# Optimization experiments

Hardware: AMD Instinct MI355X
Metric: run time of the kernel (lower is better)

Reference implementation:

```python
import jax, jax.numpy as jnp
import numpy as np

B, D, S, E = 256, 5, 30, 768
H1, H2, FF, OUT = 512, 512, 256, 2


def setup_inputs() -> dict:
    key = jax.random.key(0)
    ks = iter(jax.random.split(key, 40))

    def p(shape, scale=0.05):
        return jax.random.normal(next(ks), shape, jnp.float32) * scale

    return {
        "sentence_feats": jax.random.normal(next(ks), (B, D, S, E), jnp.float32),
        "time_feats": jax.random.uniform(next(ks), (B, D, S), jnp.float32),
        "len_tweets": jax.random.randint(next(ks), (B, D), 1, S + 1, jnp.int32),
        # TimeLSTM (lstm1)
        "Wd_w": p((H1, H1)), "Wd_b": p((H1,)),
        "Wall_w": p((4 * H1, H1)), "Wall_b": p((4 * H1,)),
        "Uall_w": p((4 * H1, E)), "Uall_b": p((4 * H1,)),
        # attn1
        "A1_W1_w": p((H1, H1)), "A1_W1_b": p((H1,)),
        "A1_W2_w": p((H1, H1)), "A1_W2_b": p((H1,)),
        "A1_V_w": p((1, H1)), "A1_V_b": p((1,)),
        # nn.LSTM (lstm2), gate order i,f,g,o
        "L2_Wih": p((4 * H2, H1)), "L2_Whh": p((4 * H2, H2)),
        "L2_bih": p((4 * H2,)), "L2_bhh": p((4 * H2,)),
        # attn2
        "A2_W1_w": p((H2, H2)), "A2_W1_b": p((H2,)),
        "A2_W2_w": p((H2, H2)), "A2_W2_b": p((H2,)),
        "A2_V_w": p((1, H2)), "A2_V_b": p((1,)),
        # head
        "lin3_w": p((FF, H2)), "lin3_b": p((FF,)),
        "lin4_w": p((OUT, FF)), "lin4_b": p((OUT,)),
    }


def _time_lstm(x, t, Wd_w, Wd_b, Wall_w, Wall_b, Uall_w, Uall_b):
    # x: (N,S,E), t: (N,S) -> o-gate outputs (N,S,H) (the torch module stacks `o`, not `h`)
    N = x.shape[0]
    H = Wd_w.shape[0]
    ux = jnp.einsum('nse,ge->nsg', x, Uall_w) + Uall_b  # (N,S,4H), hoisted out of recurrence

    def step(carry, inp):
        h, c = carry
        ux_s, t_s = inp
        c_s1 = jnp.tanh(c @ Wd_w.T + Wd_b)
        c_adj = c - c_s1 + c_s1 * t_s[:, None]
        gates = jax.nn.sigmoid(h @ Wall_w.T + Wall_b + ux_s)
        f, i, o, c_tmp = jnp.split(gates, 4, axis=1)  # all sigmoid, incl. c_tmp (as in source)
        c = f * c_adj + i * c_tmp
        h = o * jnp.tanh(c)
        return (h, c), o

    init = (jnp.zeros((N, H), x.dtype), jnp.zeros((N, H), x.dtype))
    _, os = jax.lax.scan(step, init, (ux.transpose(1, 0, 2), t.T))
    return os.transpose(1, 0, 2)  # (N,S,H)


def _std_lstm(x, Wih, Whh, bih, bhh):
    # PyTorch nn.LSTM, 1 layer, batch_first. x: (B,T,I) -> (hs (B,T,H), h_n (B,H))
    Bn = x.shape[0]
    H = Whh.shape[1]
    xi = jnp.einsum('bti,gi->btg', x, Wih) + bih + bhh  # (B,T,4H)

    def step(carry, xi_t):
        h, c = carry
        g = xi_t + h @ Whh.T
        i, f, gg, o = jnp.split(g, 4, axis=1)
        c = jax.nn.sigmoid(f) * c + jax.nn.sigmoid(i) * jnp.tanh(gg)
        h = jax.nn.sigmoid(o) * jnp.tanh(c)
        return (h, c), h

    init = (jnp.zeros((Bn, H), x.dtype), jnp.zeros((Bn, H), x.dtype))
    (h_n, _), hs = jax.lax.scan(step, init, xi.transpose(1, 0, 2))
    return hs.transpose(1, 0, 2), h_n


def _forward(sentence_feats, time_feats, Wd_w, Wd_b, Wall_w, Wall_b, Uall_w, Uall_b,
             A1_W1_w, A1_W1_b, A1_W2_w, A1_W2_b, A1_V_w, A1_V_b,
             L2_Wih, L2_Whh, L2_bih, L2_bhh,
             A2_W1_w, A2_W1_b, A2_W2_w, A2_W2_b, A2_V_w, A2_V_b,
             lin3_w, lin3_b, lin4_w, lin4_b, len_tweets):
    x = sentence_feats.transpose(1, 0, 2, 3)  # (D,B,S,E)
    t = time_feats.transpose(1, 0, 2)         # (D,B,S)
    lens = len_tweets.transpose(1, 0)          # (D,B)
    d, b, s, e = x.shape

    # run TimeLSTM over all days at once (days are independent, shared zero init)
    outs = _time_lstm(x.reshape(d * b, s, e), t.reshape(d * b, s),
                      Wd_w, Wd_b, Wall_w, Wall_b, Uall_w, Uall_b).reshape(d, b, s, H1)

    # Faithful to the source's inner loop: temp_hn ends up as the LAST batch
    # element's output at index len-1, shared across the whole batch of that day.
    idx = lens[:, -1] - 1  # (D,)
    last = jnp.take_along_axis(outs[:, -1], idx[:, None, None], axis=1)[:, 0]  # (D,H1)

    # attn1: score = V(tanh(W1(last) + W2(full))), mask by lens, softmax over S
    s1 = jnp.tanh((last @ A1_W1_w.T + A1_W1_b)[:, None, None, :]
                  + jnp.einsum('dbsh,gh->dbsg', outs, A1_W2_w) + A1_W2_b)
    score = jnp.einsum('dbsh,oh->dbso', s1, A1_V_w) + A1_V_b  # (D,B,S,1)
    mask = jnp.arange(s)[None, None, :] < lens[:, :, None]     # (D,B,S)
    score = jnp.where(mask[..., None], score, -jnp.inf)
    aw = jax.nn.softmax(score, axis=2)
    lstm1_out = jnp.sum(aw * outs, axis=2).transpose(1, 0, 2)  # (B,D,H1)

    lstm2_out, hn2 = _std_lstm(lstm1_out, L2_Wih, L2_Whh, L2_bih, L2_bhh)  # (B,D,H2),(B,H2)

    # attn2 over days
    s2 = jnp.tanh((hn2 @ A2_W1_w.T + A2_W1_b)[:, None, :]
                  + lstm2_out @ A2_W2_w.T + A2_W2_b)
    score2 = s2 @ A2_V_w.T + A2_V_b                 # (B,D,1)
    aw2 = jax.nn.softmax(score2, axis=1)
    ctx = jnp.sum(aw2 * lstm2_out, axis=1)          # (B,H2)

    h3 = jax.nn.relu(ctx @ lin3_w.T + lin3_b)       # dropout = identity (eval mode)
    return h3 @ lin4_w.T + lin4_b                   # (B,OUT)


def reference(sentence_feats, time_feats, len_tweets, Wd_w, Wd_b, Wall_w, Wall_b, Uall_w, Uall_b,
              A1_W1_w, A1_W1_b, A1_W2_w, A1_W2_b, A1_V_w, A1_V_b,
              L2_Wih, L2_Whh, L2_bih, L2_bhh,
              A2_W1_w, A2_W1_b, A2_W2_w, A2_W2_b, A2_V_w, A2_V_b,
              lin3_w, lin3_b, lin4_w, lin4_b):
    return _forward(sentence_feats, time_feats, Wd_w, Wd_b, Wall_w, Wall_b, Uall_w, Uall_b,
                    A1_W1_w, A1_W1_b, A1_W2_w, A1_W2_b, A1_V_w, A1_V_b,
                    L2_Wih, L2_Whh, L2_bih, L2_bhh,
                    A2_W1_w, A2_W1_b, A2_W2_w, A2_W2_b, A2_V_w, A2_V_b,
                    lin3_w, lin3_b, lin4_w, lin4_b, len_tweets)
```

## Files before the change

kernel.cpp:

```cpp
#include <hip/hip_runtime.h>
#include <math.h>

typedef _Float16 f16;
typedef _Float16 f16x4 __attribute__((ext_vector_type(4)));
typedef _Float16 f16x8 __attribute__((ext_vector_type(8)));
typedef float f32x4 __attribute__((ext_vector_type(4)));

#define DEV static __device__ __forceinline__

#define OFF_X16    ((size_t)0)
#define OFF_UX     ((size_t)58982400)
#define OFF_OUTS   ((size_t)216268800)
#define OFF_WD     ((size_t)255590400)
#define OFF_WALLP  ((size_t)256114688)
#define OFF_UP     ((size_t)258211840)
#define OFF_W2     ((size_t)261357568)
#define OFF_WIHP   ((size_t)261881856)
#define OFF_WHHP   ((size_t)263979008)
#define OFF_A2W1C  ((size_t)266076160)
#define OFF_A2W2C  ((size_t)266600448)
#define OFF_L3WC   ((size_t)267124736)
#define OFF_BALLP  ((size_t)267386880)
#define OFF_BIHP   ((size_t)267395072)
#define OFF_H16    ((size_t)267403264)
#define OFF_C16    ((size_t)270024704)
#define OFF_C32    ((size_t)272646144)
#define WS_NEED    ((size_t)277889024)
#define OFF_SCORE  ((size_t)0)
#define OFF_W1L    ((size_t)153600)
#define OFF_L1O32  ((size_t)163840)
#define OFF_L1O16  ((size_t)2785280)
#define OFF_XI2    ((size_t)4096000)
#define OFF_C2     ((size_t)14581760)
#define OFF_H2     ((size_t)15630336)
#define OFF_L2O32  ((size_t)16154624)
#define OFF_L2O16  ((size_t)18776064)
#define OFF_U2     ((size_t)20086784)
#define OFF_V2     ((size_t)22708224)
#define OFF_CTX16  ((size_t)23232512)
#define OFF_H3     ((size_t)23494656)
#define OFF_TFT    ((size_t)23756800)

DEV float sigf(float x) { return 1.f / (1.f + __expf(-x)); }
DEV float tanhfast(float x) { float e = __expf(2.f * x); return 1.f - 2.f / (e + 1.f); }
DEV int permrow(int c) { return (((c >> 4) & 3) << 9) | ((c >> 6) << 4) | (c & 15); }

DEV void gload16(const f16* g, f16x8* lds) {
  __builtin_amdgcn_global_load_lds((const __attribute__((address_space(1))) void*)g,
                                   (__attribute__((address_space(3))) void*)lds, 16, 0, 0);
}

DEV void gemm_core(const f16* __restrict__ A, const f16* __restrict__ Bt, int K,
                   int rowBase, int colBase, f16x8* sh, f32x4 (&acc)[4][4]) {
  const int t = threadIdx.x, lane = t & 63, w = t >> 6;
  const int wr = (w >> 1) * 64, wc = (w & 1) * 64;
  const f16* Arow = A + (size_t)rowBase * K;
  const f16* Brow = Bt + (size_t)colBase * K;
  auto stage = [&](f16x8* dstBase, const f16* src, int k0) {
#pragma unroll
    for (int i = 0; i < 4; ++i) {
      int c = i * 256 + t; int r = c >> 3; int cc = (c & 7) ^ (r & 7);
      gload16(src + (size_t)r * K + (k0 + cc * 8), dstBase + i * 256 + (t & 192));
    }
  };
  stage(sh, Arow, 0);
  stage(sh + 2048, Brow, 0);
  const int nk = K >> 6;
  for (int kt = 0; kt < nk; ++kt) {
    const int cur = kt & 1;
    if (kt + 1 < nk) {
      stage(sh + (cur ^ 1) * 1024, Arow, (kt + 1) * 64);
      stage(sh + 2048 + (cur ^ 1) * 1024, Brow, (kt + 1) * 64);
      asm volatile("s_waitcnt vmcnt(8)" ::: "memory");
    } else {
      asm volatile("s_waitcnt vmcnt(0)" ::: "memory");
    }
    __builtin_amdgcn_s_barrier();
    __builtin_amdgcn_sched_barrier(0);
    const f16x8* shA = sh + cur * 1024;
    const f16x8* shB = sh + 2048 + cur * 1024;
    const int rr = lane & 15, chb = lane >> 4;
#pragma unroll
    for (int kk = 0; kk < 2; ++kk) {
      const int ch = kk * 4 + chb;
      f16x8 af[4], bf[4];
#pragma unroll
      for (int m = 0; m < 4; ++m) { int row = wr + m * 16 + rr; af[m] = shA[row * 8 + (ch ^ (row & 7))]; }
#pragma unroll
      for (int n = 0; n < 4; ++n) { int row = wc + n * 16 + rr; bf[n] = shB[row * 8 + (ch ^ (row & 7))]; }
#pragma unroll
      for (int m = 0; m < 4; ++m)
#pragma unroll
        for (int n = 0; n < 4; ++n)
          acc[m][n] = __builtin_amdgcn_mfma_f32_16x16x32_f16(af[m], bf[n], acc[m][n], 0, 0, 0);
    }
    __builtin_amdgcn_sched_barrier(0);
    __builtin_amdgcn_s_barrier();
  }
}

DEV void gemm_core256(const f16* __restrict__ A, const f16* __restrict__ Bt, int K,
                      int rowBase, int colBase, f16x8 (&shA)[2][2048], f16x8 (&shB)[2][2048],
                      f32x4 (&acc)[8][4]) {
  const int t = threadIdx.x, lane = t & 63, w = t >> 6;
  const int wm = w >> 2, wn = w & 3;
  const f16* Arow = A + (size_t)rowBase * K;
  const f16* Brow = Bt + (size_t)colBase * K;
  auto stage = [&](f16x8* dst, const f16* src, int k0) {
#pragma unroll
    for (int i = 0; i < 4; ++i) {
      int c = i * 512 + t; int r = c >> 3; int cc = (c & 7) ^ (r & 7);
      gload16(src + (size_t)r * K + (k0 + cc * 8), dst + i * 512 + (t & 448));
    }
  };
  stage(shA[0], Arow, 0);
  stage(shB[0], Brow, 0);
  const int nk = K >> 6;
  for (int kt = 0; kt < nk; ++kt) {
    const int cur = kt & 1;
    if (kt + 1 < nk) {
      stage(shA[cur ^ 1], Arow, (kt + 1) * 64);
      stage(shB[cur ^ 1], Brow, (kt + 1) * 64);
      asm volatile("s_waitcnt vmcnt(8)" ::: "memory");
    } else {
      asm volatile("s_waitcnt vmcnt(0)" ::: "memory");
    }
    __builtin_amdgcn_s_barrier();
    __builtin_amdgcn_sched_barrier(0);
    const f16x8* pA = shA[cur];
    const f16x8* pB = shB[cur];
    const int rr = lane & 15, chb = lane >> 4;
#pragma unroll
    for (int kk = 0; kk < 2; ++kk) {
      const int ch = kk * 4 + chb;
      f16x8 bf[4];
#pragma unroll
      for (int n = 0; n < 4; ++n) { int row = wn * 64 + n * 16 + rr; bf[n] = pB[row * 8 + (ch ^ (row & 7))]; }
#pragma unroll
      for (int m = 0; m < 8; ++m) {
        int row = wm * 128 + m * 16 + rr;
        f16x8 af = pA[row * 8 + (ch ^ (row & 7))];
#pragma unroll
        for (int n = 0; n < 4; ++n)
          acc[m][n] = __builtin_amdgcn_mfma_f32_16x16x32_f16(af, bf[n], acc[m][n], 0, 0, 0);
      }
    }
    __builtin_amdgcn_sched_barrier(0);
    __builtin_amdgcn_s_barrier();
  }
}

__global__ __launch_bounds__(512, 1) void k_gemm256(const f16* __restrict__ A, const f16* __restrict__ Bt,
                                                    int K, int N, f16* __restrict__ C16) {
  __shared__ f16x8 shA[2][2048];
  __shared__ f16x8 shB[2][2048];
  const int rb = blockIdx.y * 256, cb = blockIdx.x * 256;
  f32x4 acc[8][4] = {};
  gemm_core256(A, Bt, K, rb, cb, shA, shB, acc);
  const int t = threadIdx.x, lane = t & 63, w = t >> 6;
  const int wm = w >> 2, wn = w & 3;
  const int ec = lane & 15, er = (lane >> 4) * 4;
#pragma unroll
  for (int m = 0; m < 8; ++m)
#pragma unroll
    for (int n = 0; n < 4; ++n) {
      const int c = cb + wn * 64 + n * 16 + ec;
#pragma unroll
      for (int j = 0; j < 4; ++j) {
        const int r = rb + wm * 128 + m * 16 + er + j;
        C16[(size_t)r * N + c] = (f16)acc[m][n][j];
      }
    }
}

__global__ __launch_bounds__(512, 1) void k_score2(const f16* __restrict__ outs, const f16* __restrict__ W2t,
    const float* __restrict__ W2b, const float* __restrict__ w1l, const float* __restrict__ V,
    float* __restrict__ score) {
  __shared__ f16x8 shA[2][2048];
  __shared__ f16x8 shB[2][2048];
  __shared__ float sacc[256];
  const int rb = blockIdx.y * 256, cb = blockIdx.x * 256;
  f32x4 acc[8][4] = {};
  gemm_core256(outs, W2t, 512, rb, cb, shA, shB, acc);
  const int t = threadIdx.x, lane = t & 63, w = t >> 6;
  const int wm = w >> 2, wn = w & 3;
  const int ec = lane & 15, er = (lane >> 4) * 4;
  if (t < 256) sacc[t] = 0.f;
  __syncthreads();
#pragma unroll
  for (int m = 0; m < 8; ++m)
#pragma unroll
    for (int j = 0; j < 4; ++j) {
      const int lr = wm * 128 + m * 16 + er + j;
      const int r = rb + lr;
      const int d = (r / 30) >> 8;
      float p = 0.f;
#pragma unroll
      for (int n = 0; n < 4; ++n) {
        const int c = cb + wn * 64 + n * 16 + ec;
        p += V[c] * tanhfast(acc[m][n][j] + W2b[c] + w1l[d * 512 + c]);
      }
      p += __shfl_xor(p, 1); p += __shfl_xor(p, 2); p += __shfl_xor(p, 4); p += __shfl_xor(p, 8);
      if (ec == 0) atomicAdd(&sacc[lr], p);
    }
  __syncthreads();
  if (t < 256) atomicAdd(&score[rb + t], sacc[t]);
}

template <int ACT, bool O32, bool O16>
__global__ __launch_bounds__(256, 2) void k_gemm(const f16* __restrict__ A, const f16* __restrict__ Bt,
                                                 int K, int N, const float* __restrict__ bias,
                                                 float* __restrict__ C32, f16* __restrict__ C16) {
  __shared__ f16x8 sh[4096];
  const int rb = blockIdx.y * 128, cb = blockIdx.x * 128;
  f32x4 acc[4][4] = {};
  gemm_core(A, Bt, K, rb, cb, sh, acc);
  const int t = threadIdx.x, lane = t & 63, w = t >> 6;
  const int wr = (w >> 1) * 64, wc = (w & 1) * 64, ec = lane & 15, er = (lane >> 4) * 4;
#pragma unroll
  for (int m = 0; m < 4; ++m)
#pragma unroll
    for (int n = 0; n < 4; ++n) {
      const int c = cb + wc + n * 16 + ec;
      const float bv = bias ? bias[c] : 0.f;
#pragma unroll
      for (int j = 0; j < 4; ++j) {
        const int r = rb + wr + m * 16 + er + j;
        float v = acc[m][n][j] + bv;
        if (ACT == 3) v = fmaxf(v, 0.f);
        if (O32) C32[(size_t)r * N + c] = v;
        if (O16) C16[(size_t)r * N + c] = (f16)v;
      }
    }
}

__global__ __launch_bounds__(256, 1) void k_stepf(
    const f16* __restrict__ hin, const f16* __restrict__ cin16, const float* __restrict__ cin32,
    const f16* __restrict__ Wallp, const f16* __restrict__ Wd16,
    const f16* __restrict__ ux, const float* __restrict__ ballp, const float* __restrict__ Wd_b,
    const float* __restrict__ tft,
    float* __restrict__ cout32, f16* __restrict__ cout16, f16* __restrict__ hout,
    f16* __restrict__ outs, int s) {
  __shared__ f16x8 shA[2048];
  __shared__ f16x8 shB[2048];
  __shared__ f16x8 shC[2048];
  __shared__ f16x8 shD[512];
  __shared__ f16x8 shU[2048];
  __shared__ f16x8 shE[1024];
  const int t = threadIdx.x, lane = t & 63, w = t >> 6;
  const int rb = ((int)blockIdx.x >> 4) * 128;
  const int cg = (int)blockIdx.x & 15;
  const int wr = (w >> 1) * 64, wc = (w & 1) * 64;
  const int rr = lane & 15, chb = lane >> 4;
  const int ec = lane & 15, er = (lane >> 4) * 4;
  const int h = cg * 32 + (w & 1) * 16 + ec;
  const int hcol = (w & 1) * 16 + ec;
  const f16* Ah = hin + (size_t)rb * 512;
  const f16* Ac = cin16 + (size_t)rb * 512;
  const f16* Bw = Wallp + (size_t)cg * 128 * 512;
  const f16* Bd = Wd16 + (size_t)cg * 32 * 512;
  float bW[4];
#pragma unroll
  for (int n = 0; n < 4; ++n) bW[n] = ballp[cg * 128 + wc + n * 16 + ec];
  const float bD = Wd_b[h];
  const f16* shUf = (const f16*)shU;
  const float* shEf = (const float*)shE;
  const int kbase = (wc >> 3) + (ec >> 3);
  f32x4 acc[4][4] = {};
  f32x4 acc2[4] = {};

  auto stage128 = [&](f16x8* dstBase, const f16* src, int k0) {
#pragma unroll
    for (int i = 0; i < 4; ++i) {
      int c = i * 256 + t; int r = c >> 3; int cc = (c & 7) ^ (r & 7);
      gload16(src + (size_t)r * 512 + (k0 + cc * 8), dstBase + i * 256 + (t & 192));
    }
  };
  auto stage32 = [&](f16x8* dstBase, const f16* src, int k0) {
    const int r = t >> 3; const int cc = (t & 7) ^ (r & 7);
    gload16(src + (size_t)r * 512 + (k0 + cc * 8), dstBase + (t & 192));
  };
  auto stageU = [&]() {
#pragma unroll
    for (int i = 0; i < 8; ++i) {
      int c = i * 256 + t; int lr = c >> 4; int k = c & 15;
      int klog = k ^ (((lr >> 2) & 3) << 1);
      gload16(ux + ((size_t)(rb + lr) * 30 + s) * 2048 + cg * 128 + klog * 8,
              shU + i * 256 + (t & 192));
    }
  };
  auto stageE = [&]() {
#pragma unroll
    for (int i = 0; i < 4; ++i) {
      int c = i * 256 + t; int lr = c >> 3; int k = c & 7;
      int klog = k ^ (((lr >> 2) & 1) << 2);
      gload16((const f16*)(cin32 + (size_t)(rb + lr) * 512 + cg * 32 + klog * 4),
              shE + i * 256 + (t & 192));
    }
  };

  if (s == 0) {
    stageU();
    stageE();
    asm volatile("s_waitcnt vmcnt(0)" ::: "memory");
    __builtin_amdgcn_s_barrier();
  } else {
    stage128(shA, Ah, 0);
    stage128(shB, Bw, 0);
    stage128(shC, Ac, 0);
    stage32(shD, Bd, 0);
    stageU();
    stageE();
    for (int kt = 0; kt < 8; ++kt) {
      const int cur = kt & 1;
      if (kt < 7) {
        stage128(shA + (cur ^ 1) * 1024, Ah, (kt + 1) * 64);
        stage128(shB + (cur ^ 1) * 1024, Bw, (kt + 1) * 64);
        stage128(shC + (cur ^ 1) * 1024, Ac, (kt + 1) * 64);
        stage32(shD + (cur ^ 1) * 256, Bd, (kt + 1) * 64);
        asm volatile("s_waitcnt vmcnt(13)" ::: "memory");
      } else {
        asm volatile("s_waitcnt vmcnt(0)" ::: "memory");
      }
      __builtin_amdgcn_s_barrier();
      __builtin_amdgcn_sched_barrier(0);
      const f16x8* pA = shA + cur * 1024;
      const f16x8* pB = shB + cur * 1024;
      const f16x8* pC = shC + cur * 1024;
      const f16x8* pD = shD + cur * 256;
#pragma unroll
      for (int kk = 0; kk < 2; ++kk) {
        const int ch = kk * 4 + chb;
        f16x8 af[4], bf[4], cf[4], df;
#pragma unroll
        for (int m = 0; m < 4; ++m) {
          const int row = wr + m * 16 + rr;
          af[m] = pA[row * 8 + (ch ^ (row & 7))];
          cf[m] = pC[row * 8 + (ch ^ (row & 7))];
        }
#pragma unroll
        for (int n = 0; n < 4; ++n) { const int row = wc + n * 16 + rr; bf[n] = pB[row * 8 + (ch ^ (row & 7))]; }
        { const int row = (w & 1) * 16 + rr; df = pD[row * 8 + (ch ^ (row & 7))]; }
#pragma unroll
        for (int m = 0; m < 4; ++m) {
#pragma unroll
          for (int n = 0; n < 4; ++n)
            acc[m][n] = __builtin_amdgcn_mfma_f32_16x16x32_f16(af[m], bf[n], acc[m][n], 0, 0, 0);
          acc2[m] = __builtin_amdgcn_mfma_f32_16x16x32_f16(cf[m], df, acc2[m], 0, 0, 0);
        }
      }
      __builtin_amdgcn_sched_barrier(0);
      __builtin_amdgcn_s_barrier();
    }
  }

#pragma unroll
  for (int m = 0; m < 4; ++m)
#pragma unroll
    for (int j = 0; j < 4; ++j) {
      const int lr = wr + m * 16 + er + j;
      const int r = rb + lr;
      const float tv = tft[s * 1280 + r];
      const int sU = ((lr >> 2) & 3) << 1;
      const float u0 = (float)shUf[(lr * 16 + ((kbase + 0) ^ sU)) * 8 + (ec & 7)];
      const float u1 = (float)shUf[(lr * 16 + ((kbase + 2) ^ sU)) * 8 + (ec & 7)];
      const float u2v = (float)shUf[(lr * 16 + ((kbase + 4) ^ sU)) * 8 + (ec & 7)];
      const float u3 = (float)shUf[(lr * 16 + ((kbase + 6) ^ sU)) * 8 + (ec & 7)];
      const float p0 = acc[m][0][j] + bW[0] + u0;
      const float p1 = acc[m][1][j] + bW[1] + u1;
      const float p2 = acc[m][2][j] + bW[2] + u2v;
      const float p3 = acc[m][3][j] + bW[3] + u3;
      const float f = sigf(p0), i = sigf(p1), o = sigf(p2), ct = sigf(p3);
      const float cs = tanhfast(acc2[m][j] + bD);
      const int sE = ((lr >> 2) & 1) << 2;
      const float c_old = shEf[(lr * 8 + ((hcol >> 2) ^ sE)) * 4 + (hcol & 3)];
      const float cadj = c_old - cs + cs * tv;
      const float cn = f * cadj + i * ct;
      cout32[(size_t)r * 512 + h] = cn;
      cout16[(size_t)r * 512 + h] = (f16)cn;
      hout[(size_t)r * 512 + h] = (f16)(o * tanhfast(cn));
      outs[((size_t)r * 30 + s) * 512 + h] = (f16)o;
    }
}

__global__ __launch_bounds__(256, 2) void k_l2step(const f16* __restrict__ hin, const f16* __restrict__ Whhp,
    const float* __restrict__ xi2, const float* __restrict__ cin, float* __restrict__ cout,
    f16* __restrict__ hout, float* __restrict__ l2o32, f16* __restrict__ l2o16, int ts) {
  __shared__ f16x8 sh[4096];
  const int rb = (blockIdx.x >> 4) * 128, cg = blockIdx.x & 15;
  f32x4 acc[4][4] = {};
  gemm_core(hin, Whhp, 512, rb, cg * 128, sh, acc);
  const int t = threadIdx.x, lane = t & 63, w = t >> 6;
  const int wr = (w >> 1) * 64, wc = (w & 1) * 64, ec = lane & 15, er = (lane >> 4) * 4;
  const int h = cg * 32 + (w & 1) * 16 + ec;
#pragma unroll
  for (int m = 0; m < 4; ++m)
#pragma unroll
    for (int j = 0; j < 4; ++j) {
      const int r = rb + wr + m * 16 + er + j;
      const size_t xb = ((size_t)r * 5 + ts) * 2048 + cg * 128 + wc + ec;
      const float p0 = acc[m][0][j] + xi2[xb];
      const float p1 = acc[m][1][j] + xi2[xb + 16];
      const float p2 = acc[m][2][j] + xi2[xb + 32];
      const float p3 = acc[m][3][j] + xi2[xb + 48];
      const float ii = sigf(p0), ff = sigf(p1), gg = tanhfast(p2), oo = sigf(p3);
      const float cn = ff * cin[(size_t)r * 512 + h] + ii * gg;
      const float hn = oo * tanhfast(cn);
      cout[(size_t)r * 512 + h] = cn;
      hout[(size_t)r * 512 + h] = (f16)hn;
      const size_t ob = ((size_t)r * 5 + ts) * 512 + h;
      l2o32[ob] = hn;
      l2o16[ob] = (f16)hn;
    }
}

__global__ __launch_bounds__(256) void k_w1last(const f16* __restrict__ outs, const int* __restrict__ lens,
                                                const float* __restrict__ W1, const float* __restrict__ W1b,
                                                float* __restrict__ w1l) {
  __shared__ float lastv[512];
  const int d = blockIdx.x;
  const int idx = lens[255 * 5 + d] - 1;
  const size_t row = ((size_t)(d * 256 + 255) * 30 + idx) * 512;
  for (int h = threadIdx.x; h < 512; h += 256) lastv[h] = (float)outs[row + h];
  __syncthreads();
  for (int h = threadIdx.x; h < 512; h += 256) {
    const float* wr = W1 + (size_t)h * 512;
    float p = W1b[h];
    for (int k = 0; k < 512; ++k) p += lastv[k] * wr[k];
    w1l[d * 512 + h] = p;
  }
}

__global__ __launch_bounds__(256) void k_attn1(const float* __restrict__ score, const f16* __restrict__ outs,
                                               const int* __restrict__ lens,
                                               float* __restrict__ l1o32, f16* __restrict__ l1o16) {
  __shared__ float saw[32];
  const int n = blockIdx.x;
  const int d = n >> 8, b = n & 255;
  const int len = lens[b * 5 + d];
  const int t = threadIdx.x, lane = t & 63, w = t >> 6;
  if (w == 0) {
    const bool valid = lane < len;
    float sc = valid ? score[(size_t)n * 30 + lane] : -INFINITY;
    float mx = sc;
#pragma unroll
    for (int off = 32; off > 0; off >>= 1) mx = fmaxf(mx, __shfl_xor(mx, off));
    float e = valid ? __expf(sc - mx) : 0.f;
    float sm = e;
#pragma unroll
    for (int off = 32; off > 0; off >>= 1) sm += __shfl_xor(sm, off);
    if (lane < 30) saw[lane] = e / sm;
  }
  __syncthreads();
  for (int h = t; h < 512; h += 256) {
    float acc = 0.f;
    for (int s = 0; s < len; ++s) acc += saw[s] * (float)outs[((size_t)n * 30 + s) * 512 + h];
    const size_t o = ((size_t)b * 5 + d) * 512 + h;
    l1o32[o] = acc;
    l1o16[o] = (f16)acc;
  }
}

__global__ __launch_bounds__(256, 2) void k_uv(const f16* __restrict__ l2o16, const f16* __restrict__ A2W2c,
    const f16* __restrict__ h2fin, const f16* __restrict__ A2W1c,
    const float* __restrict__ bu, const float* __restrict__ bv,
    float* __restrict__ u2, float* __restrict__ v2) {
  __shared__ f16x8 sh[4096];
  const int bid = blockIdx.x;
  const f16* A; const f16* B; const float* bias; float* out; int rb, cb;
  if (bid < 40) { A = l2o16; B = A2W2c; bias = bu; out = u2; rb = (bid >> 2) * 128; cb = (bid & 3) * 128; }
  else { int b2 = bid - 40; A = h2fin; B = A2W1c; bias = bv; out = v2; rb = (b2 >> 2) * 128; cb = (b2 & 3) * 128; }
  f32x4 acc[4][4] = {};
  gemm_core(A, B, 512, rb, cb, sh, acc);
  const int t = threadIdx.x, lane = t & 63, w = t >> 6;
  const int wr = (w >> 1) * 64, wc = (w & 1) * 64, ec = lane & 15, er = (lane >> 4) * 4;
#pragma unroll
  for (int m = 0; m < 4; ++m)
#pragma unroll
    for (int n = 0; n < 4; ++n) {
      const int c = cb + wc + n * 16 + ec;
      const float bvv = bias[c];
#pragma unroll
      for (int j = 0; j < 4; ++j) out[(size_t)(rb + wr + m * 16 + er + j) * 512 + c] = acc[m][n][j] + bvv;
    }
}

__global__ __launch_bounds__(256) void k_attn2(const float* __restrict__ u2, const float* __restrict__ v2,
                                               const float* __restrict__ l2o, const float* __restrict__ V2,
                                               const float* __restrict__ V2b, f16* __restrict__ ctx16) {
  __shared__ float ssc[8];
  __shared__ float saw[8];
  const int b = blockIdx.x;
  const int t = threadIdx.x, lane = t & 63, w = t >> 6;
  for (int tt = w; tt < 5; tt += 4) {
    const float* ur = u2 + ((size_t)b * 5 + tt) * 512;
    const float* vr = v2 + (size_t)b * 512;
    float p = 0.f;
#pragma unroll
    for (int j = 0; j < 8; ++j) { int h = lane * 8 + j; p += V2[h] * tanhfast(ur[h] + vr[h]); }
#pragma unroll
    for (int off = 32; off > 0; off >>= 1) p += __shfl_down(p, off);
    if (lane == 0) ssc[tt] = p + V2b[0];
  }
  __syncthreads();
  if (w == 0) {
    const bool valid = lane < 5;
    float sc = valid ? ssc[lane] : -INFINITY;
    float mx = sc;
#pragma unroll
    for (int off = 32; off > 0; off >>= 1) mx = fmaxf(mx, __shfl_xor(mx, off));
    float e = valid ? __expf(sc - mx) : 0.f;
    float sm = e;
#pragma unroll
    for (int off = 32; off > 0; off >>= 1) sm += __shfl_xor(sm, off);
    if (valid) saw[lane] = e / sm;
  }
  __syncthreads();
  for (int h = t; h < 512; h += 256) {
    float a = 0.f;
#pragma unroll
    for (int tt = 0; tt < 5; ++tt) a += saw[tt] * l2o[((size_t)b * 5 + tt) * 512 + h];
    ctx16[(size_t)b * 512 + h] = (f16)a;
  }
}

__global__ __launch_bounds__(256) void k_final(const float* __restrict__ h3, const float* __restrict__ W4,
                                               const float* __restrict__ b4, float* __restrict__ out) {
  const int idx = blockIdx.x * 256 + threadIdx.x;
  const int b = idx >> 1, o = idx & 1;
  const float* hr = h3 + b * 256;
  const float* wr = W4 + o * 256;
  float p = b4[o];
  for (int j = 0; j < 256; ++j) p += hr[j] * wr[j];
  out[idx] = p;
}

__global__ __launch_bounds__(256) void k_castx(const float* __restrict__ sf, f16* __restrict__ x16) {
  const int total = 7372800;
  for (int e = blockIdx.x * 256 + threadIdx.x; e < total; e += gridDim.x * 256) {
    const int row = e / 192, k = e - row * 192;
    const int b = row / 150, rem = row - b * 150;
    const int d = rem / 30, s = rem - d * 30;
    const int orow = (d * 256 + b) * 30 + s;
    const float4 v = ((const float4*)sf)[e];
    f16x4 o = {(f16)v.x, (f16)v.y, (f16)v.z, (f16)v.w};
    ((f16x4*)x16)[(size_t)orow * 192 + k] = o;
  }
}

struct WPArgs { const float* src[9]; f16* dst[9]; int k4[9]; int cnt4[9]; int perm[9]; };
__global__ __launch_bounds__(256) void k_castwp(WPArgs a) {
  int g = blockIdx.x * 256 + threadIdx.x;
#pragma unroll
  for (int si = 0; si < 9; ++si) {
    if (g < a.cnt4[si]) {
      const int K4 = a.k4[si];
      const int c = g / K4, k = g - c * K4;
      const int srow = a.perm[si] ? permrow(c) : c;
      const float4 v = ((const float4*)a.src[si])[(size_t)srow * K4 + k];
      f16x4 o = {(f16)v.x, (f16)v.y, (f16)v.z, (f16)v.w};
      ((f16x4*)a.dst[si])[(size_t)c * K4 + k] = o;
      return;
    }
    g -= a.cnt4[si];
  }
}

__global__ __launch_bounds__(256) void k_zero(f16* h16a, f16* c16a, float* c32a,
    float* ballp, float* bihp, const float* Wall_b, const float* Uall_b,
    const float* bih, const float* bhh, float* tft, const float* tf,
    float* score, const float* Vb, f16* h2a, float* c2a) {
  const int i = blockIdx.x * 256 + threadIdx.x;
  if (i < 655360) { h16a[i] = (f16)0.f; c16a[i] = (f16)0.f; c32a[i] = 0.f; }
  if (i < 2048) {
    const int p = permrow(i);
    ballp[i] = Wall_b[p] + Uall_b[p];
    bihp[i] = bih[p] + bhh[p];
  }
  if (i < 38400) {
    const int s = i / 1280, r = i - s * 1280;
    const int d = r >> 8, b = r & 255;
    tft[i] = tf[((size_t)b * 5 + d) * 30 + s];
    score[i] = Vb[0];
  }
  if (i < 131072) { h2a[i] = (f16)0.f; c2a[i] = 0.f; }
}

extern "C" void kernel_launch(void* const* d_in, const int* in_sizes, int n_in,
                              void* d_out, int out_size, void* d_ws, size_t ws_size,
                              hipStream_t stream) {
  const float* sf     = (const float*)d_in[0];
  const float* tf     = (const float*)d_in[1];
  const int*   lens   = (const int*)d_in[2];
  const float* Wd_w   = (const float*)d_in[3];
  const float* Wd_b   = (const float*)d_in[4];
  const float* Wall_w = (const float*)d_in[5];
  const float* Wall_b = (const float*)d_in[6];
  const float* Uall_w = (const float*)d_in[7];
  const float* Uall_b = (const float*)d_in[8];
  const float* A1W1   = (const float*)d_in[9];
  const float* A1W1b  = (const float*)d_in[10];
  const float* A1W2   = (const float*)d_in[11];
  const float* A1W2b  = (const float*)d_in[12];
  const float* A1V    = (const float*)d_in[13];
  const float* A1Vb   = (const float*)d_in[14];
  const float* Wih    = (const float*)d_in[15];
  const float* Whh    = (const float*)d_in[16];
  const float* bih    = (const float*)d_in[17];
  const float* bhh    = (const float*)d_in[18];
  const float* A2W1   = (const float*)d_in[19];
  const float* A2W1b  = (const float*)d_in[20];
  const float* A2W2   = (const float*)d_in[21];
  const float* A2W2b  = (const float*)d_in[22];
  const float* A2V    = (const float*)d_in[23];
  const float* A2Vb   = (const float*)d_in[24];
  const float* L3w    = (const float*)d_in[25];
  const float* L3b    = (const float*)d_in[26];
  const float* L4w    = (const float*)d_in[27];
  const float* L4b    = (const float*)d_in[28];

  if (ws_size < WS_NEED) return;
  char* ws = (char*)d_ws;
  f16*   x16    = (f16*)(ws + OFF_X16);
  f16*   ux16   = (f16*)(ws + OFF_UX);
  f16*   outs16 = (f16*)(ws + OFF_OUTS);
  f16*   Wd16   = (f16*)(ws + OFF_WD);
  f16*   Wallp  = (f16*)(ws + OFF_WALLP);
  f16*   U16p   = (f16*)(ws + OFF_UP);
  f16*   W216   = (f16*)(ws + OFF_W2);
  f16*   Wihp   = (f16*)(ws + OFF_WIHP);
  f16*   Whhp   = (f16*)(ws + OFF_WHHP);
  f16*   A2W116 = (f16*)(ws + OFF_A2W1C);
  f16*   A2W216 = (f16*)(ws + OFF_A2W2C);
  f16*   L316   = (f16*)(ws + OFF_L3WC);
  float* ballp  = (float*)(ws + OFF_BALLP);
  float* bihp   = (float*)(ws + OFF_BIHP);
  f16*   h16b[2]  = {(f16*)(ws + OFF_H16), (f16*)(ws + OFF_H16 + 1310720)};
  f16*   c16b[2]  = {(f16*)(ws + OFF_C16), (f16*)(ws + OFF_C16 + 1310720)};
  float* c32b[2]  = {(float*)(ws + OFF_C32), (float*)(ws + OFF_C32 + 2621440)};
  float* score  = (float*)(ws + OFF_SCORE);
  float* w1l    = (float*)(ws + OFF_W1L);
  float* l1o32  = (float*)(ws + OFF_L1O32);
  f16*   l1o16  = (f16*)(ws + OFF_L1O16);
  float* xi2    = (float*)(ws + OFF_XI2);
  float* c2b[2] = {(float*)(ws + OFF_C2), (float*)(ws + OFF_C2 + 524288)};
  f16*   h2b[2] = {(f16*)(ws + OFF_H2), (f16*)(ws + OFF_H2 + 262144)};
  float* l2o32  = (float*)(ws + OFF_L2O32);
  f16*   l2o16  = (f16*)(ws + OFF_L2O16);
  float* u2     = (float*)(ws + OFF_U2);
  float* v2     = (float*)(ws + OFF_V2);
  f16*   ctx16  = (f16*)(ws + OFF_CTX16);
  float* h3     = (float*)(ws + OFF_H3);
  float* tft    = (float*)(ws + OFF_TFT);

  k_castx<<<2048, 256, 0, stream>>>(sf, x16);
  WPArgs wa;
  wa.src[0] = Wd_w;   wa.dst[0] = Wd16;   wa.k4[0] = 128; wa.cnt4[0] = 65536;  wa.perm[0] = 0;
  wa.src[1] = A1W2;   wa.dst[1] = W216;   wa.k4[1] = 128; wa.cnt4[1] = 65536;  wa.perm[1] = 0;
  wa.src[2] = A2W1;   wa.dst[2] = A2W116; wa.k4[2] = 128; wa.cnt4[2] = 65536;  wa.perm[2] = 0;
  wa.src[3] = A2W2;   wa.dst[3] = A2W216; wa.k4[3] = 128; wa.cnt4[3] = 65536;  wa.perm[3] = 0;
  wa.src[4] = L3w;    wa.dst[4] = L316;   wa.k4[4] = 128; wa.cnt4[4] = 32768;  wa.perm[4] = 0;
  wa.src[5] = Wall_w; wa.dst[5] = Wallp;  wa.k4[5] = 128; wa.cnt4[5] = 262144; wa.perm[5] = 1;
  wa.src[6] = Uall_w; wa.dst[6] = U16p;   wa.k4[6] = 192; wa.cnt4[6] = 393216; wa.perm[6] = 1;
  wa.src[7] = Wih;    wa.dst[7] = Wihp;   wa.k4[7] = 128; wa.cnt4[7] = 262144; wa.perm[7] = 1;
  wa.src[8] = Whh;    wa.dst[8] = Whhp;   wa.k4[8] = 128; wa.cnt4[8] = 262144; wa.perm[8] = 1;
  k_castwp<<<5760, 256, 0, stream>>>(wa);

  k_gemm256<<<dim3(8, 150), 512, 0, stream>>>(x16, U16p, 768, 2048, ux16);

  k_zero<<<2560, 256, 0, stream>>>(h16b[0], c16b[0], c32b[0], ballp, bihp, Wall_b, Uall_b, bih, bhh,
                                   tft, tf, score, A1Vb, h2b[0], c2b[0]);

  for (int s = 0; s < 30; ++s) {
    const int pi = s & 1, po = pi ^ 1;
    k_stepf<<<160, 256, 0, stream>>>(h16b[pi], c16b[pi], c32b[pi], Wallp, Wd16, ux16, ballp, Wd_b, tft,
                                     c32b[po], c16b[po], h16b[po], outs16, s);
  }

  k_w1last<<<5, 256, 0, stream>>>(outs16, lens, A1W1, A1W1b, w1l);
  k_score2<<<dim3(2, 150), 512, 0, stream>>>(outs16, W216, A1W2b, w1l, A1V, score);
  k_attn1<<<1280, 256, 0, stream>>>(score, outs16, lens, l1o32, l1o16);

  k_gemm<0, true, false><<<dim3(16, 10), 256, 0, stream>>>(l1o16, Wihp, 512, 2048, bihp, xi2, nullptr);
  for (int ts = 0; ts < 5; ++ts) {
    const int pi = ts & 1, po = pi ^ 1;
    k_l2step<<<32, 256, 0, stream>>>(h2b[pi], Whhp, xi2, c2b[pi], c2b[po], h2b[po], l2o32, l2o16, ts);
  }

  k_uv<<<48, 256, 0, stream>>>(l2o16, A2W216, h2b[1], A2W116, A2W2b, A2W1b, u2, v2);
  k_attn2<<<256, 256, 0, stream>>>(u2, v2, l2o32, A2V, A2Vb, ctx16);

  k_gemm<3, true, false><<<dim3(2, 2), 256, 0, stream>>>(ctx16, L316, 512, 256, L3b, h3, nullptr);
  k_final<<<2, 256, 0, stream>>>(h3, L4w, L4b, (float*)d_out);
}
```

Before: 1.016 ms.

## Overlap input projection GEMM with TimeLSTM recurrence steps

The x·Uᵀ projection is no longer computed in full before the recurrence. The input is re-laid out time-major, only the first two timesteps' slabs are computed up front, and each recurrence launch adds 160 extra blocks that compute slab s+2 alongside the step. This hides most of the large projection GEMM behind the latency-bound, underfilled recurrence kernels. The cost is shared LDS allocation, heavier launches, and moving the tft/score/h2 buffers to avoid aliasing with the workspace.

```diff
diff --git a/kernel.cpp b/kernel.cpp
--- a/kernel.cpp
+++ b/kernel.cpp
@@ -25,8 +25,9 @@
 #define OFF_H16    ((size_t)267403264)
 #define OFF_C16    ((size_t)270024704)
 #define OFF_C32    ((size_t)272646144)
-#define WS_NEED    ((size_t)277889024)
-#define OFF_SCORE  ((size_t)0)
+#define OFF_TFTN   ((size_t)277889024)
+#define OFF_SCOREN (OFF_TFTN + 153600)
+#define WS_NEED    (OFF_SCOREN + 153600)
 #define OFF_W1L    ((size_t)153600)
 #define OFF_L1O32  ((size_t)163840)
 #define OFF_L1O16  ((size_t)2785280)
@@ -39,7 +40,6 @@
 #define OFF_V2     ((size_t)22708224)
 #define OFF_CTX16  ((size_t)23232512)
 #define OFF_H3     ((size_t)23494656)
-#define OFF_TFT    ((size_t)23756800)
 
 DEV float sigf(float x) { return 1.f / (1.f + __expf(-x)); }
 DEV float tanhfast(float x) { float e = __expf(2.f * x); return 1.f - 2.f / (e + 1.f); }
@@ -234,31 +234,55 @@
     }
 }
 
-__global__ __launch_bounds__(256, 1) void k_stepf(
+__global__ __launch_bounds__(256, 1) void k_stepm(
     const f16* __restrict__ hin, const f16* __restrict__ cin16, const float* __restrict__ cin32,
     const f16* __restrict__ Wallp, const f16* __restrict__ Wd16,
     const f16* __restrict__ ux, const float* __restrict__ ballp, const float* __restrict__ Wd_b,
     const float* __restrict__ tft,
     float* __restrict__ cout32, f16* __restrict__ cout16, f16* __restrict__ hout,
-    f16* __restrict__ outs, int s) {
-  __shared__ f16x8 shA[2048];
-  __shared__ f16x8 shB[2048];
-  __shared__ f16x8 shC[2048];
-  __shared__ f16x8 shD[512];
-  __shared__ f16x8 shU[2048];
-  __shared__ f16x8 shE[1024];
-  const int t = threadIdx.x, lane = t & 63, w = t >> 6;
-  const int rb = ((int)blockIdx.x >> 4) * 128;
-  const int cg = (int)blockIdx.x & 15;
+    f16* __restrict__ outs,
+    const f16* __restrict__ x16s, const f16* __restrict__ U16p, f16* __restrict__ uxout, int s) {
+  __shared__ f16x8 shAll[9728];
+  const int bid = (int)blockIdx.x;
+  const int t = threadIdx.x, lane = t & 63, w = t >> 6;
   const int wr = (w >> 1) * 64, wc = (w & 1) * 64;
+  const int ec = lane & 15, er = (lane >> 4) * 4;
+
+  if (bid >= 160) {
+    const int q = bid - 160;
+    const int slab = s + 2;
+    const int rbu = (q >> 4) * 128, cbu = (q & 15) * 128;
+    f32x4 acc[4][4] = {};
+    gemm_core(x16s + (size_t)slab * 1280 * 768, U16p, 768, rbu, cbu, shAll, acc);
+    f16* C = uxout + (size_t)slab * 1280 * 2048;
+#pragma unroll
+    for (int m = 0; m < 4; ++m)
+#pragma unroll
+      for (int n = 0; n < 4; ++n) {
+        const int c = cbu + wc + n * 16 + ec;
+#pragma unroll
+        for (int j = 0; j < 4; ++j)
+          C[(size_t)(rbu + wr + m * 16 + er + j) * 2048 + c] = (f16)acc[m][n][j];
+      }
+    return;
+  }
+
+  f16x8* shA = shAll;
+  f16x8* shB = shAll + 2048;
+  f16x8* shC = shAll + 4096;
+  f16x8* shD = shAll + 6144;
+  f16x8* shU = shAll + 6656;
+  f16x8* shE = shAll + 8704;
+  const int rb = (bid >> 4) * 128;
+  const int cg = bid & 15;
   const int rr = lane & 15, chb = lane >> 4;
-  const int ec = lane & 15, er = (lane >> 4) * 4;
   const int h = cg * 32 + (w & 1) * 16 + ec;
   const int hcol = (w & 1) * 16 + ec;
   const f16* Ah = hin + (size_t)rb * 512;
   const f16* Ac = cin16 + (size_t)rb * 512;
   const f16* Bw = Wallp + (size_t)cg * 128 * 512;
   const f16* Bd = Wd16 + (size_t)cg * 32 * 512;
+  const f16* uxs = ux + (size_t)s * 1280 * 2048;
   float bW[4];
 #pragma unroll
   for (int n = 0; n < 4; ++n) bW[n] = ballp[cg * 128 + wc + n * 16 + ec];
@@ -285,8 +309,7 @@
     for (int i = 0; i < 8; ++i) {
       int c = i * 256 + t; int lr = c >> 4; int k = c & 15;
       int klog = k ^ (((lr >> 2) & 3) << 1);
-      gload16(ux + ((size_t)(rb + lr) * 30 + s) * 2048 + cg * 128 + klog * 8,
-              shU + i * 256 + (t & 192));
+      gload16(uxs + (size_t)(rb + lr) * 2048 + cg * 128 + klog * 8, shU + i * 256 + (t & 192));
     }
   };
   auto stageE = [&]() {
@@ -535,16 +558,16 @@
   out[idx] = p;
 }
 
-__global__ __launch_bounds__(256) void k_castx(const float* __restrict__ sf, f16* __restrict__ x16) {
+__global__ __launch_bounds__(256) void k_castx(const float* __restrict__ sf, f16* __restrict__ x16s) {
   const int total = 7372800;
   for (int e = blockIdx.x * 256 + threadIdx.x; e < total; e += gridDim.x * 256) {
     const int row = e / 192, k = e - row * 192;
     const int b = row / 150, rem = row - b * 150;
     const int d = rem / 30, s = rem - d * 30;
-    const int orow = (d * 256 + b) * 30 + s;
+    const int orow = s * 1280 + d * 256 + b;
     const float4 v = ((const float4*)sf)[e];
     f16x4 o = {(f16)v.x, (f16)v.y, (f16)v.z, (f16)v.w};
-    ((f16x4*)x16)[(size_t)orow * 192 + k] = o;
+    ((f16x4*)x16s)[(size_t)orow * 192 + k] = o;
   }
 }
 
@@ -569,7 +592,7 @@
 __global__ __launch_bounds__(256) void k_zero(f16* h16a, f16* c16a, float* c32a,
     float* ballp, float* bihp, const float* Wall_b, const float* Uall_b,
     const float* bih, const float* bhh, float* tft, const float* tf,
-    float* score, const float* Vb, f16* h2a, float* c2a) {
+    float* score, const float* Vb) {
   const int i = blockIdx.x * 256 + threadIdx.x;
   if (i < 655360) { h16a[i] = (f16)0.f; c16a[i] = (f16)0.f; c32a[i] = 0.f; }
   if (i < 2048) {
@@ -583,6 +606,10 @@
     tft[i] = tf[((size_t)b * 5 + d) * 30 + s];
     score[i] = Vb[0];
   }
+}
+
+__global__ __launch_bounds__(256) void k_init2(f16* h2a, float* c2a) {
+  const int i = blockIdx.x * 256 + threadIdx.x;
   if (i < 131072) { h2a[i] = (f16)0.f; c2a[i] = 0.f; }
 }
 
@@ -621,7 +648,7 @@
 
   if (ws_size < WS_NEED) return;
   char* ws = (char*)d_ws;
-  f16*   x16    = (f16*)(ws + OFF_X16);
+  f16*   x16s   = (f16*)(ws + OFF_X16);
   f16*   ux16   = (f16*)(ws + OFF_UX);
   f16*   outs16 = (f16*)(ws + OFF_OUTS);
   f16*   Wd16   = (f16*)(ws + OFF_WD);
@@ -638,7 +665,8 @@
   f16*   h16b[2]  = {(f16*)(ws + OFF_H16), (f16*)(ws + OFF_H16 + 1310720)};
   f16*   c16b[2]  = {(f16*)(ws + OFF_C16), (f16*)(ws + OFF_C16 + 1310720)};
   float* c32b[2]  = {(float*)(ws + OFF_C32), (float*)(ws + OFF_C32 + 2621440)};
-  float* score  = (float*)(ws + OFF_SCORE);
+  float* tft    = (float*)(ws + OFF_TFTN);
+  float* score  = (float*)(ws + OFF_SCOREN);
   float* w1l    = (float*)(ws + OFF_W1L);
   float* l1o32  = (float*)(ws + OFF_L1O32);
   f16*   l1o16  = (f16*)(ws + OFF_L1O16);
@@ -651,9 +679,8 @@
   float* v2     = (float*)(ws + OFF_V2);
   f16*   ctx16  = (f16*)(ws + OFF_CTX16);
   float* h3     = (float*)(ws + OFF_H3);
-  float* tft    = (float*)(ws + OFF_TFT);
-
-  k_castx<<<2048, 256, 0, stream>>>(sf, x16);
+
+  k_castx<<<2048, 256, 0, stream>>>(sf, x16s);
   WPArgs wa;
   wa.src[0] = Wd_w;   wa.dst[0] = Wd16;   wa.k4[0] = 128; wa.cnt4[0] = 65536;  wa.perm[0] = 0;
   wa.src[1] = A1W2;   wa.dst[1] = W216;   wa.k4[1] = 128; wa.cnt4[1] = 65536;  wa.perm[1] = 0;
@@ -665,17 +692,20 @@
   wa.src[7] = Wih;    wa.dst[7] = Wihp;   wa.k4[7] = 128; wa.cnt4[7] = 262144; wa.perm[7] = 1;
   wa.src[8] = Whh;    wa.dst[8] = Whhp;   wa.k4[8] = 128; wa.cnt4[8] = 262144; wa.perm[8] = 1;
   k_castwp<<<5760, 256, 0, stream>>>(wa);
-
-  k_gemm256<<<dim3(8, 150), 512, 0, stream>>>(x16, U16p, 768, 2048, ux16);
-
   k_zero<<<2560, 256, 0, stream>>>(h16b[0], c16b[0], c32b[0], ballp, bihp, Wall_b, Uall_b, bih, bhh,
-                                   tft, tf, score, A1Vb, h2b[0], c2b[0]);
+                                   tft, tf, score, A1Vb);
+
+  k_gemm256<<<dim3(8, 10), 512, 0, stream>>>(x16s, U16p, 768, 2048, ux16);
 
   for (int s = 0; s < 30; ++s) {
     const int pi = s & 1, po = pi ^ 1;
-    k_stepf<<<160, 256, 0, stream>>>(h16b[pi], c16b[pi], c32b[pi], Wallp, Wd16, ux16, ballp, Wd_b, tft,
-                                     c32b[po], c16b[po], h16b[po], outs16, s);
-  }
+    const int nb = (s <= 27) ? 320 : 160;
+    k_stepm<<<nb, 256, 0, stream>>>(h16b[pi], c16b[pi], c32b[pi], Wallp, Wd16, ux16, ballp, Wd_b, tft,
+                                    c32b[po], c16b[po], h16b[po], outs16,
+                                    x16s, U16p, ux16, s);
+  }
+
+  k_init2<<<512, 256, 0, stream>>>(h2b[0], c2b[0]);
 
   k_w1last<<<5, 256, 0, stream>>>(outs16, lens, A1W1, A1W1b, w1l);
   k_score2<<<dim3(2, 150), 512, 0, stream>>>(outs16, W216, A1W2b, w1l, A1V, score);
```

Result: faster. 946.9 us (-6.8%).
